# Performance work log

Hardware: AMD Instinct MI355X
Metric: run time of the kernel (lower is better)

Reference implementation:

```python
import jax, jax.numpy as jnp
import numpy as np
import math

NUM_HEADS = 16
TOPK = 64
EMBED = 1024

def setup_inputs() -> dict:
    key = jax.random.key(0)
    ks = jax.random.split(key, 11)
    b, s, e = 2, 2048, EMBED
    scale = 1.0 / math.sqrt(e)
    inp = {
        'q': jax.random.normal(ks[0], (b, s, e), dtype=jnp.float32),
        'k': jax.random.normal(ks[1], (b, s, e), dtype=jnp.float32),
        'v': jax.random.normal(ks[2], (b, s, e), dtype=jnp.float32),
        'Wq': jax.random.normal(ks[3], (e, e), dtype=jnp.float32) * scale,
        'bq': jnp.zeros((e,), dtype=jnp.float32),
        'Wk': jax.random.normal(ks[4], (e, e), dtype=jnp.float32) * scale,
        'bk': jnp.zeros((e,), dtype=jnp.float32),
        'Wv': jax.random.normal(ks[5], (e, e), dtype=jnp.float32) * scale,
        'bv': jnp.zeros((e,), dtype=jnp.float32),
        'Wo': jax.random.normal(ks[6], (e, e), dtype=jnp.float32) * scale,
        'bo': jnp.zeros((e,), dtype=jnp.float32),
    }
    return inp

def _topk_attention(Q, K, V, topk):
    # Q,K,V: (b, h, s, d)
    d = Q.shape[-1]
    scores = jnp.einsum('bhqd,bhkd->bhqk', Q, K) / jnp.sqrt(jnp.asarray(d, Q.dtype))
    topk_scores, topk_idx = jax.lax.top_k(scores, topk)  # (b,h,s,topk)
    probs = jax.nn.softmax(topk_scores, axis=-1)
    # gather V rows per (b,h): V_bh[idx] -> (s, topk, d); avoids (b,h,s,s,d) expand
    gather = jax.vmap(jax.vmap(lambda Vbh, idx: Vbh[idx]))
    sel = gather(V, topk_idx)  # (b,h,s,topk,d)
    return jnp.einsum('bhqk,bhqkd->bhqd', probs, sel)

def reference(q, k, v, Wq, bq, Wk, bk, Wv, bv, Wo, bo):
    b, s, e = q.shape
    h = NUM_HEADS
    d = e // h
    # NOTE: original torch code reshapes (b, s, e) -> (b, h, s, d) directly (no transpose)
    Q = (q @ Wq.T + bq).reshape(b, h, s, d)
    K = (k @ Wk.T + bk).reshape(b, h, s, d)
    V = (v @ Wv.T + bv).reshape(b, h, s, d)
    attn = _topk_attention(Q, K, V, TOPK)  # (b,h,s,d)
    out = attn.reshape(b, s, e)
    return out @ Wo.T + bo
```

## Files before the change

### kernel.cpp

```cpp
#include <hip/hip_runtime.h>
#include <stdint.h>

using u8  = unsigned char;
using s8  = signed char;
using u16 = unsigned short;
using u32 = unsigned int;
using u64 = unsigned long long;

typedef int   v4i __attribute__((ext_vector_type(4)));
typedef float v4f __attribute__((ext_vector_type(4)));
typedef short v8s __attribute__((ext_vector_type(8)));

__device__ __forceinline__ u16 f2bf(float f){
  u32 u = __builtin_bit_cast(u32, f);
  u32 r = (u + 0x7FFFu + ((u >> 16) & 1u)) >> 16;
  return (u16)r;
}
__device__ __forceinline__ float bf2f(u16 b){
  u32 u = ((u32)b) << 16;
  return __builtin_bit_cast(float, u);
}

__global__ __launch_bounds__(256) void quant_digits(
    const float* __restrict__ in, s8* __restrict__ dig, int n, float scale, float clampv)
{
  int t = blockIdx.x * 256 + threadIdx.x;
  int n8 = n >> 3;
  if (t >= n8) return;
  const float4* inv = (const float4*)in;
  float4 a = inv[2*t], b = inv[2*t+1];
  float xs[8] = {a.x,a.y,a.z,a.w,b.x,b.y,b.z,b.w};
  u64 p0=0,p1=0,p2=0,p3=0;
#pragma unroll
  for (int j=0;j<8;j++){
    float xv = fminf(fmaxf(xs[j], -clampv), clampv);
    int X = (int)rintf(xv * scale);
    int d0 = (int)(s8)(X & 255); X = (X - d0) >> 8;
    int d1 = (int)(s8)(X & 255); X = (X - d1) >> 8;
    int d2 = (int)(s8)(X & 255); X = (X - d2) >> 8;
    int d3 = X;
    p0 |= ((u64)(u8)(s8)d0) << (8*j);
    p1 |= ((u64)(u8)(s8)d1) << (8*j);
    p2 |= ((u64)(u8)(s8)d2) << (8*j);
    p3 |= ((u64)(u8)(s8)d3) << (8*j);
  }
  u64* o = (u64*)dig;
  size_t np8 = (size_t)n8;
  o[t] = p0; o[np8 + t] = p1; o[2*np8 + t] = p2; o[3*np8 + t] = p3;
}

#define MFMA_I8(c, a, b) asm volatile("v_mfma_i32_16x16x64_i8 %0, %1, %2, %0" : "+v"(c) : "v"(a), "v"(b))

__global__ __launch_bounds__(256) void gemm_i8(
    const s8* __restrict__ Ad, const s8* __restrict__ Wd, const float* __restrict__ bias,
    double* __restrict__ Cd, u16* __restrict__ Cb)
{
  __shared__ alignas(16) s8 As[4][64][80];
  __shared__ alignas(16) s8 Bs[4][64][80];
  const int i0 = blockIdx.x * 64, o0 = blockIdx.y * 64;
  const int t = threadIdx.x, w = t >> 6, lane = t & 63;
  const int wr = w >> 1, wc = w & 1, l15 = lane & 15, lg = lane >> 4;
  const int sr = (t >> 2) & 63, sc = (t & 3) << 4;
  const size_t APL = 4194304, WPL = 1048576;

  v4i acc[2][2][4];
#pragma unroll
  for (int tr = 0; tr < 2; ++tr)
#pragma unroll
    for (int tc = 0; tc < 2; ++tc)
#pragma unroll
      for (int c = 0; c < 4; ++c) acc[tr][tc][c] = (v4i){0,0,0,0};

  for (int kt = 0; kt < 16; ++kt){
#pragma unroll
    for (int p = 0; p < 4; ++p){
      int4 av = *(const int4*)(Ad + (size_t)p*APL + (size_t)(i0+sr)*1024 + kt*64 + sc);
      *(int4*)&As[p][sr][sc] = av;
      int4 bv = *(const int4*)(Wd + (size_t)p*WPL + (size_t)(o0+sr)*1024 + kt*64 + sc);
      *(int4*)&Bs[p][sr][sc] = bv;
    }
    __syncthreads();
    v4i af[2][4], bf[2][4];
#pragma unroll
    for (int tr = 0; tr < 2; ++tr)
#pragma unroll
      for (int p = 0; p < 4; ++p){
        af[tr][p] = *(const v4i*)&As[p][wr*32 + tr*16 + l15][lg*16];
        bf[tr][p] = *(const v4i*)&Bs[p][wc*32 + tr*16 + l15][lg*16];
      }
#pragma unroll
    for (int tr = 0; tr < 2; ++tr)
#pragma unroll
      for (int tc = 0; tc < 2; ++tc){
        MFMA_I8(acc[tr][tc][0], af[tr][0], bf[tc][3]);
        MFMA_I8(acc[tr][tc][0], af[tr][1], bf[tc][2]);
        MFMA_I8(acc[tr][tc][0], af[tr][2], bf[tc][1]);
        MFMA_I8(acc[tr][tc][0], af[tr][3], bf[tc][0]);
        MFMA_I8(acc[tr][tc][1], af[tr][1], bf[tc][3]);
        MFMA_I8(acc[tr][tc][1], af[tr][2], bf[tc][2]);
        MFMA_I8(acc[tr][tc][1], af[tr][3], bf[tc][1]);
        MFMA_I8(acc[tr][tc][2], af[tr][2], bf[tc][3]);
        MFMA_I8(acc[tr][tc][2], af[tr][3], bf[tc][2]);
        MFMA_I8(acc[tr][tc][3], af[tr][3], bf[tc][3]);
      }
    __syncthreads();
  }
#pragma unroll
  for (int tr = 0; tr < 2; ++tr)
#pragma unroll
    for (int tc = 0; tc < 2; ++tc){
      const int oc = o0 + wc*32 + tc*16 + l15;
      const double bv = (double)bias[oc];
#pragma unroll
      for (int e = 0; e < 4; ++e){
        double val = (double)acc[tr][tc][0][e]*0x1p-35 + (double)acc[tr][tc][1][e]*0x1p-27
                   + (double)acc[tr][tc][2][e]*0x1p-19 + (double)acc[tr][tc][3][e]*0x1p-11 + bv;
        int orow = i0 + wr*32 + tr*16 + lg*4 + e;
        size_t idx = (size_t)orow*1024 + oc;
        Cd[idx] = val;
        Cb[idx] = f2bf((float)val);
      }
    }
}

template<int ABF16, int OUTBF>
__global__ __launch_bounds__(256) void gemm_bf16k(
    const void* __restrict__ Ap, const float* __restrict__ W, const float* __restrict__ bias,
    void* __restrict__ C)
{
  __shared__ alignas(16) u16 As[64][72];
  __shared__ alignas(16) u16 Bs[64][72];
  const int i0 = blockIdx.x * 64, o0 = blockIdx.y * 64;
  const int t = threadIdx.x, w = t >> 6, lane = t & 63;
  const int wr = w >> 1, wc = w & 1, l15 = lane & 15, lg = lane >> 4;
  const int sr = t >> 2, sc = (t & 3) << 4;

  v4f acc[2][2];
#pragma unroll
  for (int tr = 0; tr < 2; ++tr)
#pragma unroll
    for (int tc = 0; tc < 2; ++tc) acc[tr][tc] = (v4f){0.f,0.f,0.f,0.f};

  for (int kt = 0; kt < 16; ++kt){
    if (ABF16){
      const u16* A = (const u16*)Ap;
      v8s x0 = *(const v8s*)(A + (size_t)(i0+sr)*1024 + kt*64 + sc);
      v8s x1 = *(const v8s*)(A + (size_t)(i0+sr)*1024 + kt*64 + sc + 8);
      *(v8s*)&As[sr][sc] = x0;
      *(v8s*)&As[sr][sc+8] = x1;
    } else {
      const float* A = (const float*)Ap;
      v8s pk0, pk1;
#pragma unroll
      for (int h = 0; h < 2; ++h){
        const float4 y0 = *(const float4*)(A + (size_t)(i0+sr)*1024 + kt*64 + sc + h*8);
        const float4 y1 = *(const float4*)(A + (size_t)(i0+sr)*1024 + kt*64 + sc + h*8 + 4);
        v8s& pk = h ? pk1 : pk0;
        pk[0]=(short)f2bf(y0.x); pk[1]=(short)f2bf(y0.y); pk[2]=(short)f2bf(y0.z); pk[3]=(short)f2bf(y0.w);
        pk[4]=(short)f2bf(y1.x); pk[5]=(short)f2bf(y1.y); pk[6]=(short)f2bf(y1.z); pk[7]=(short)f2bf(y1.w);
      }
      *(v8s*)&As[sr][sc] = pk0;
      *(v8s*)&As[sr][sc+8] = pk1;
    }
    {
      v8s pk0, pk1;
#pragma unroll
      for (int h = 0; h < 2; ++h){
        const float4 y0 = *(const float4*)(W + (size_t)(o0+sr)*1024 + kt*64 + sc + h*8);
        const float4 y1 = *(const float4*)(W + (size_t)(o0+sr)*1024 + kt*64 + sc + h*8 + 4);
        v8s& pk = h ? pk1 : pk0;
        pk[0]=(short)f2bf(y0.x); pk[1]=(short)f2bf(y0.y); pk[2]=(short)f2bf(y0.z); pk[3]=(short)f2bf(y0.w);
        pk[4]=(short)f2bf(y1.x); pk[5]=(short)f2bf(y1.y); pk[6]=(short)f2bf(y1.z); pk[7]=(short)f2bf(y1.w);
      }
      *(v8s*)&Bs[sr][sc] = pk0;
      *(v8s*)&Bs[sr][sc+8] = pk1;
    }
    __syncthreads();
    v8s a[2][2], b[2][2];
#pragma unroll
    for (int tr = 0; tr < 2; ++tr)
#pragma unroll
      for (int ks = 0; ks < 2; ++ks){
        a[tr][ks] = *(const v8s*)&As[wr*32 + tr*16 + l15][ks*32 + lg*8];
        b[tr][ks] = *(const v8s*)&Bs[wc*32 + tr*16 + l15][ks*32 + lg*8];
      }
#pragma unroll
    for (int tr = 0; tr < 2; ++tr)
#pragma unroll
      for (int tc = 0; tc < 2; ++tc){
        acc[tr][tc] = __builtin_amdgcn_mfma_f32_16x16x32_bf16(a[tr][0], b[tc][0], acc[tr][tc], 0, 0, 0);
        acc[tr][tc] = __builtin_amdgcn_mfma_f32_16x16x32_bf16(a[tr][1], b[tc][1], acc[tr][tc], 0, 0, 0);
      }
    __syncthreads();
  }
#pragma unroll
  for (int tr = 0; tr < 2; ++tr)
#pragma unroll
    for (int tc = 0; tc < 2; ++tc){
      const int oc = o0 + wc*32 + tc*16 + l15;
      const float bvv = bias[oc];
#pragma unroll
      for (int e = 0; e < 4; ++e){
        int orow = i0 + wr*32 + tr*16 + lg*4 + e;
        size_t idx = (size_t)orow*1024 + oc;
        if (OUTBF) ((u16*)C)[idx] = f2bf(acc[tr][tc][e] + bvv);
        else       ((float*)C)[idx] = acc[tr][tc][e] + bvv;
      }
    }
}

#define CCAP 192
__global__ __launch_bounds__(512, 4) void attn_topk(
    const u16* __restrict__ Qb, const u16* __restrict__ Kb,
    const double* __restrict__ Qd, const double* __restrict__ Kd,
    const u16* __restrict__ Vb, u16* __restrict__ Ab, u32* __restrict__ flags)
{
  __shared__ u32 candL[32*CCAP];
  __shared__ u32 selpL[16*64];
  __shared__ int cntA[32];

  const int lid = blockIdx.y * 64 + blockIdx.x;
  const int bh  = (lid & 7) * 4 + (lid >> 9);
  const int qb  = (lid >> 3) & 63;
  const size_t base = (size_t)(bh >> 4) * 2097152 + (size_t)(bh & 15) * 131072;
  const int q0 = qb * 32;
  const int tid = threadIdx.x, w = tid >> 6, lane = tid & 63;
  const int l15 = lane & 15, lg = lane >> 4;
  const u64 ltmask = (1ull << lane) - 1ull;

  if (tid < 32) cntA[tid] = 0;
  __syncthreads();

  const v4f vzero = {0.f,0.f,0.f,0.f};
  float nrmA, nrmB;
  {
    const size_t qoffA = base + (size_t)(q0 + l15)*64 + lg*8;
    v8s aA0 = *(const v8s*)(Qb + qoffA);
    v8s aA1 = *(const v8s*)(Qb + qoffA + 32);
    v8s aB0 = *(const v8s*)(Qb + qoffA + 1024);
    v8s aB1 = *(const v8s*)(Qb + qoffA + 1024 + 32);

    nrmA = 0.f; nrmB = 0.f;
#pragma unroll
    for (int m = 0; m < 8; ++m){
      float xA0 = bf2f((u16)aA0[m]), xA1 = bf2f((u16)aA1[m]);
      float xB0 = bf2f((u16)aB0[m]), xB1 = bf2f((u16)aB1[m]);
      nrmA = fmaf(xA0,xA0,nrmA); nrmA = fmaf(xA1,xA1,nrmA);
      nrmB = fmaf(xB0,xB0,nrmB); nrmB = fmaf(xB1,xB1,nrmB);
    }
    nrmA += __shfl_xor(nrmA,16); nrmA += __shfl_xor(nrmA,32);
    nrmB += __shfl_xor(nrmB,16); nrmB += __shfl_xor(nrmB,32);
    float T0A[4], T0B[4];
#pragma unroll
    for (int e = 0; e < 4; ++e){
      T0A[e] = 0.2f * sqrtf(__shfl(nrmA, lg*4 + e));
      T0B[e] = 0.2f * sqrtf(__shfl(nrmB, lg*4 + e));
    }

    const u16* Kw = Kb + base + (size_t)(w*256 + l15)*64 + lg*8;
    v8s b0 = *(const v8s*)(Kw);
    v8s b1 = *(const v8s*)(Kw + 32);

    auto step = [&](int kt, v8s b0c, v8s b1c){
      v4f sA = __builtin_amdgcn_mfma_f32_16x16x32_bf16(aA0, b0c, vzero, 0,0,0);
      sA = __builtin_amdgcn_mfma_f32_16x16x32_bf16(aA1, b1c, sA, 0,0,0);
      v4f sB = __builtin_amdgcn_mfma_f32_16x16x32_bf16(aB0, b0c, vzero, 0,0,0);
      sB = __builtin_amdgcn_mfma_f32_16x16x32_bf16(aB1, b1c, sB, 0,0,0);
      const u32 col = (u32)(w*256 + kt*16 + l15);
#pragma unroll
      for (int e = 0; e < 4; ++e){
        float sc = sA[e]*0.125f;
        if (sc >= T0A[e]){
          int row = lg*4 + e;
          int pos = atomicAdd(&cntA[row], 1);
          if (pos < CCAP) candL[row*CCAP + pos] = ((u32)f2bf(sc)<<16) | col;
        }
        float sc2 = sB[e]*0.125f;
        if (sc2 >= T0B[e]){
          int row = 16 + lg*4 + e;
          int pos = atomicAdd(&cntA[row], 1);
          if (pos < CCAP) candL[row*CCAP + pos] = ((u32)f2bf(sc2)<<16) | col;
        }
      }
    };

    for (int kt = 0; kt < 15; ++kt){
      v8s n0 = *(const v8s*)(Kw + (size_t)(kt+1)*1024);
      v8s n1 = *(const v8s*)(Kw + (size_t)(kt+1)*1024 + 32);
      step(kt, b0, b1);
      b0 = n0; b1 = n1;
    }
    step(15, b0, b1);
  }
  __syncthreads();

  for (int pass = 0; pass < 2; ++pass){
    const int R0 = pass*16 + w*2;
    const float nrmP0 = (pass == 0) ? nrmA : nrmB;
    u32 pk0[2], pk1[2], pk2[2], cstore[2], tv[2];
    bool fail[2];

#pragma unroll
    for (int rr = 0; rr < 2; ++rr){
      const int R = R0 + rr;
      int craw = cntA[R];
      fail[rr] = (craw > CCAP);
      cstore[rr] = (u32)(craw > CCAP ? CCAP : craw);
#pragma unroll
      for (int s = 0; s < 3; ++s){
        u32 idx = (u32)(64*s + lane);
        u32 val = (idx < cstore[rr]) ? candL[R*CCAP + idx] : 0u;
        if (s == 0) pk0[rr] = val; else if (s == 1) pk1[rr] = val; else pk2[rr] = val;
      }
      tv[rr] = 0u;
    }

    for (int bit = 14; bit >= 0; --bit){
#pragma unroll
      for (int rr = 0; rr < 2; ++rr){
        u32 tt = tv[rr] | (1u << bit);
        int c = (int)__popcll(__ballot((pk0[rr] >> 16) >= tt))
              + (int)__popcll(__ballot((pk1[rr] >> 16) >= tt))
              + (int)__popcll(__ballot((pk2[rr] >> 16) >= tt));
        if (c >= 64) tv[rr] = tt;
      }
    }

    int na[2], nb[2];
#pragma unroll
    for (int rr = 0; rr < 2; ++rr){
      const int R = R0 + rr;
      const int Rl = R & 15;
      float t64f = bf2f((u16)tv[rr]);
      float T0R = 0.2f * sqrtf(__shfl(nrmP0, R & 15));
      float thi = t64f + 0.052f, tlo = t64f - 0.052f;
      int a_ = 0, b_ = 0;
#pragma unroll
      for (int s = 0; s < 3; ++s){
        u32 pkv = (s == 0) ? pk0[rr] : ((s == 1) ? pk1[rr] : pk2[rr]);
        bool act = (u32)(64*s + lane) < cstore[rr];
        float v = bf2f((u16)(pkv >> 16));
        bool aut = act && (v > thi);
        bool ban = act && !aut && (v >= tlo);
        u64 ma = __ballot(aut);
        if (aut){
          int pos = a_ + (int)__popcll(ma & ltmask);
          if (pos < 64) selpL[Rl*64 + pos] = pkv;
        }
        a_ += (int)__popcll(ma);
        u64 mb = __ballot(ban);
        if (ban){
          int pos = b_ + (int)__popcll(mb & ltmask);
          if (pos < 64) candL[R*CCAP + pos] = pkv;
        }
        b_ += (int)__popcll(mb);
      }
      bool fl = fail[rr] || (t64f < T0R + 0.055f) || (t64f >= 3.98f) || (b_ > 64);
      fail[rr] = fl;
      if (lane == 0) flags[bh*2048 + q0 + R] = fl ? 1u : 0u;
      na[rr] = fl ? 64 : (a_ > 64 ? 64 : a_);
      nb[rr] = fl ? 0  : b_;
    }
    asm volatile("s_waitcnt lgkmcnt(0)" ::: "memory");
    __builtin_amdgcn_sched_barrier(0);

    const double* Kdh = Kd + base;
    const double* Qdh = Qd + base + (size_t)q0*64;
    u32 bpk[2];
#pragma unroll
    for (int rr = 0; rr < 2; ++rr)
      bpk[rr] = (lane < nb[rr]) ? candL[(R0+rr)*CCAP + lane] : 0u;
    double ac0[2] = {0,0}, ac1[2] = {0,0};
#pragma unroll 4
    for (int j = 0; j < 32; ++j){
#pragma unroll
      for (int rr = 0; rr < 2; ++rr){
        double2 kv = ((const double2*)(Kdh + (size_t)(bpk[rr] & 0x7FFu)*64))[j];
        double2 qv = ((const double2*)(Qdh + (size_t)(R0+rr)*64))[j];
        ac0[rr] = fma(qv.x, kv.x, ac0[rr]);
        ac1[rr] = fma(qv.y, kv.y, ac1[rr]);
      }
    }
    double mv[2]; int mi[2];
#pragma unroll
    for (int rr = 0; rr < 2; ++rr){
      mv[rr] = (lane < nb[rr]) ? (ac0[rr] + ac1[rr]) : -1.0e300;
      mi[rr] = (lane < nb[rr]) ? (int)(bpk[rr] & 0x7FFu) : 0x7FFFFFFF;
    }
    int maxnb = nb[0] > nb[1] ? nb[0] : nb[1];
    int rank[2] = {0,0};
    for (int j = 0; j < maxnb; ++j){
#pragma unroll
      for (int rr = 0; rr < 2; ++rr){
        double ov = __shfl(mv[rr], j); int oi = __shfl(mi[rr], j);
        rank[rr] += (ov > mv[rr] || (ov == mv[rr] && oi < mi[rr])) ? 1 : 0;
      }
    }
#pragma unroll
    for (int rr = 0; rr < 2; ++rr){
      int need = 64 - na[rr]; if (need > nb[rr]) need = nb[rr];
      if (lane < nb[rr] && rank[rr] < need)
        selpL[((R0+rr) & 15)*64 + na[rr] + rank[rr]] = bpk[rr];
    }
    asm volatile("s_waitcnt lgkmcnt(0)" ::: "memory");
    __builtin_amdgcn_sched_barrier(0);

    u32 sidx[2]; float scv[2], pp[2];
#pragma unroll
    for (int rr = 0; rr < 2; ++rr){
      u32 pr = selpL[((R0+rr) & 15)*64 + lane];
      sidx[rr] = pr & 0x7FFu;
      scv[rr] = __builtin_bit_cast(float, pr & 0xFFFF0000u);
    }
#pragma unroll
    for (int rr = 0; rr < 2; ++rr){
      float mx = scv[rr];
#pragma unroll
      for (int off = 32; off; off >>= 1) mx = fmaxf(mx, __shfl_xor(mx, off));
      float p = expf(scv[rr] - mx);
      float Z = p;
#pragma unroll
      for (int off = 32; off; off >>= 1) Z += __shfl_xor(Z, off);
      pp[rr] = p / Z;
    }
    u64 myp0 = ((u64)__builtin_bit_cast(u32, pp[0]) << 32) | (u64)sidx[0];
    u64 myp1 = ((u64)__builtin_bit_cast(u32, pp[1]) << 32) | (u64)sidx[1];

    const int h = lane >> 5, dl = lane & 31;
    float u0[2] = {0,0}, u1[2] = {0,0};
#pragma unroll 4
    for (int j = 0; j < 64; j += 2){
      u64 pr0 = __shfl(myp0, j + h);
      u64 pr1 = __shfl(myp1, j + h);
#pragma unroll
      for (int rr = 0; rr < 2; ++rr){
        u64 pr = (rr == 0) ? pr0 : pr1;
        float pv = __builtin_bit_cast(float, (u32)(pr >> 32));
        u32 vv = *(const u32*)(Vb + base + (size_t)((u32)pr & 0x7FFu)*64 + 2*dl);
        u0[rr] = fmaf(pv, bf2f((u16)(vv & 0xFFFFu)), u0[rr]);
        u1[rr] = fmaf(pv, bf2f((u16)(vv >> 16)),     u1[rr]);
      }
    }
#pragma unroll
    for (int rr = 0; rr < 2; ++rr){
      u0[rr] += __shfl_xor(u0[rr], 32);
      u1[rr] += __shfl_xor(u1[rr], 32);
    }
    if (lane < 32){
#pragma unroll
      for (int rr = 0; rr < 2; ++rr){
        u32 o = (u32)f2bf(u0[rr]) | ((u32)f2bf(u1[rr]) << 16);
        *(u32*)(Ab + base + (size_t)(q0 + R0 + rr)*64 + 2*dl) = o;
      }
    }
  }
}

__global__ __launch_bounds__(256) void attn_fallback(
    const u32* __restrict__ flags, const double* __restrict__ Qd,
    const double* __restrict__ Kd, const u16* __restrict__ Vb,
    u16* __restrict__ Ab)
{
  __shared__ double ktileL[4][16*64];
  __shared__ double valsL[2048];
  __shared__ double qlds[64];
  __shared__ double selvL[64];
  __shared__ int    seliL[64];
  __shared__ float  ppL[64];
  __shared__ float  ovL[4][64];
  __shared__ double redv[4];
  __shared__ int    redi[4];
  __shared__ double bcv;
  __shared__ int    bci;
  __shared__ u32    mskL;

  const int blk = blockIdx.x;
  const int tid = threadIdx.x, w = tid >> 6, lane = tid & 63;

  if (tid == 0){
    u32 m = 0;
    for (int i = 0; i < 16; ++i) m |= (flags[blk*16 + i] ? 1u : 0u) << i;
    mskL = m;
  }
  __syncthreads();
  const u32 msk = mskL;
  if (msk == 0u) return;

  for (int i = 0; i < 16; ++i){
    if (!((msk >> i) & 1u)) continue;
    const int g = blk*16 + i;
    const int bh = g >> 11, qrow = g & 2047;
    const size_t base = (size_t)(bh >> 4)*2097152 + (size_t)(bh & 15)*131072;
    if (tid < 64) qlds[tid] = Qd[base + (size_t)qrow*64 + tid];
    __syncthreads();

    double* ktw = ktileL[w];
    const int gg = lane >> 4, r = lane & 15;
    for (int t = 0; t < 32; ++t){
      const int k0 = w*512 + t*16;
#pragma unroll
      for (int r2 = 0; r2 < 16; ++r2)
        ktw[r2*64 + ((lane + r2) & 63)] = Kd[base + (size_t)(k0 + r2)*64 + lane];
      double p = 0.0;
#pragma unroll
      for (int dd = 0; dd < 16; ++dd){
        int d = gg*16 + dd;
        p = fma(qlds[d], ktw[r*64 + ((d + r) & 63)], p);
      }
      p += __shfl_xor(p, 16);
      p += __shfl_xor(p, 32);
      if (lane < 16) valsL[k0 + lane] = p * 0.125;
    }
    __syncthreads();

    double myv[8];
#pragma unroll
    for (int m2 = 0; m2 < 8; ++m2) myv[m2] = valsL[tid*8 + m2];

    double pvv = 1.0e300; int pii = -1;
    for (int step = 0; step < 64; ++step){
      double bv = -1.0e300; int bi = 0x7FFFFFFF;
#pragma unroll
      for (int m2 = 0; m2 < 8; ++m2){
        double vv = myv[m2]; int col = tid*8 + m2;
        bool after = (vv < pvv) || (vv == pvv && col > pii);
        bool bet = after && (vv > bv || (vv == bv && col < bi));
        bv = bet ? vv : bv; bi = bet ? col : bi;
      }
#pragma unroll
      for (int off = 32; off; off >>= 1){
        double ov = __shfl_xor(bv, off); int oi = __shfl_xor(bi, off);
        bool tk = (ov > bv) || (ov == bv && oi < bi);
        bv = tk ? ov : bv; bi = tk ? oi : bi;
      }
      if (lane == 0){ redv[w] = bv; redi[w] = bi; }
      __syncthreads();
      if (tid == 0){
        double fv = redv[0]; int fi = redi[0];
#pragma unroll
        for (int x = 1; x < 4; ++x){
          bool tk = (redv[x] > fv) || (redv[x] == fv && redi[x] < fi);
          fv = tk ? redv[x] : fv; fi = tk ? redi[x] : fi;
        }
        bcv = fv; bci = fi; selvL[step] = fv; seliL[step] = fi;
      }
      __syncthreads();
      pvv = bcv; pii = bci;
    }

    if (w == 0){
      float sc = (float)selvL[lane];
      float mx = sc;
#pragma unroll
      for (int off = 32; off; off >>= 1) mx = fmaxf(mx, __shfl_xor(mx, off));
      float p = expf(sc - mx);
      float Z = p;
#pragma unroll
      for (int off = 32; off; off >>= 1) Z += __shfl_xor(Z, off);
      ppL[lane] = p / Z;
    }
    __syncthreads();

    float o = 0.f;
#pragma unroll
    for (int j = 0; j < 16; ++j){
      int jj = w*16 + j;
      o = fmaf(ppL[jj], bf2f(Vb[base + (size_t)seliL[jj]*64 + lane]), o);
    }
    ovL[w][lane] = o;
    __syncthreads();
    if (w == 0){
      float oo = (ovL[0][lane] + ovL[1][lane]) + (ovL[2][lane] + ovL[3][lane]);
      Ab[base + (size_t)qrow*64 + lane] = f2bf(oo);
    }
    __syncthreads();
  }
}

extern "C" void kernel_launch(void* const* d_in, const int* in_sizes, int n_in,
                              void* d_out, int out_size, void* d_ws, size_t ws_size,
                              hipStream_t stream)
{
  (void)in_sizes; (void)n_in; (void)out_size; (void)ws_size;
  const float* q  = (const float*)d_in[0];
  const float* k  = (const float*)d_in[1];
  const float* v  = (const float*)d_in[2];
  const float* Wq = (const float*)d_in[3];
  const float* bq = (const float*)d_in[4];
  const float* Wk = (const float*)d_in[5];
  const float* bk = (const float*)d_in[6];
  const float* Wv = (const float*)d_in[7];
  const float* bv = (const float*)d_in[8];
  const float* Wo = (const float*)d_in[9];
  const float* bo = (const float*)d_in[10];

  char* ws = (char*)d_ws;
  const size_t MB = 1048576;
  double* Qd  = (double*)(ws);
  double* Kd  = (double*)(ws + 32*MB);
  u16*    Qb  = (u16*)  (ws + 64*MB);
  u16*    Kb  = (u16*)  (ws + 72*MB);
  u16*    Abf = (u16*)  (ws + 80*MB);
  s8*     dact= (s8*)   (ws + 88*MB);
  u16*    Vbf = (u16*)  (ws + 88*MB);
  s8*     dw  = (s8*)   (ws + 104*MB);
  u32*    flg = (u32*)  (ws + 104*MB);

  quant_digits<<<2048, 256, 0, stream>>>(q,  dact, 4194304, 134217728.0f, 7.75f);
  quant_digits<<<512,  256, 0, stream>>>(Wq, dw,   1048576, 4294967296.0f, 0.2495f);
  gemm_i8<<<dim3(64, 16), 256, 0, stream>>>(dact, dw, bq, Qd, Qb);
  quant_digits<<<2048, 256, 0, stream>>>(k,  dact, 4194304, 134217728.0f, 7.75f);
  quant_digits<<<512,  256, 0, stream>>>(Wk, dw,   1048576, 4294967296.0f, 0.2495f);
  gemm_i8<<<dim3(64, 16), 256, 0, stream>>>(dact, dw, bk, Kd, Kb);
  gemm_bf16k<0,1><<<dim3(64, 16), 256, 0, stream>>>(v, Wv, bv, Vbf);
  attn_topk<<<dim3(64, 32), 512, 0, stream>>>(Qb, Kb, Qd, Kd, Vbf, Abf, flg);
  attn_fallback<<<4096, 256, 0, stream>>>(flg, Qd, Kd, Vbf, Abf);
  gemm_bf16k<1,0><<<dim3(64, 16), 256, 0, stream>>>(Abf, Wo, bo, d_out);
}
```

Measured before the change: 588.4 us.

## Process 64 query rows per attention block to reuse each K tile more

The top-k attention kernel now handles 64 query rows per block instead of 32, holding four Q fragments in registers and running four MFMA groups against each loaded K tile. The grid is halved and the selection phase loops over four passes. The aim is to amortise K loads over more queries. In exchange it uses more registers and LDS (the candidate buffer grows even with a slightly smaller per-row cap), which may cut occupancy, and the smaller cap could push more rows into the fallback path.

```diff
diff --git a/kernel.cpp b/kernel.cpp
--- a/kernel.cpp
+++ b/kernel.cpp
@@ -209,52 +209,51 @@
     }
 }
 
-#define CCAP 192
+#define CCAP 184
 __global__ __launch_bounds__(512, 4) void attn_topk(
     const u16* __restrict__ Qb, const u16* __restrict__ Kb,
     const double* __restrict__ Qd, const double* __restrict__ Kd,
     const u16* __restrict__ Vb, u16* __restrict__ Ab, u32* __restrict__ flags)
 {
-  __shared__ u32 candL[32*CCAP];
+  __shared__ u32 candL[64*CCAP];
   __shared__ u32 selpL[16*64];
-  __shared__ int cntA[32];
-
-  const int lid = blockIdx.y * 64 + blockIdx.x;
-  const int bh  = (lid & 7) * 4 + (lid >> 9);
-  const int qb  = (lid >> 3) & 63;
+  __shared__ int cntA[64];
+
+  const int lid = blockIdx.y * 32 + blockIdx.x;
+  const int bh  = (lid & 7) * 4 + (lid >> 8);
+  const int qb  = (lid >> 3) & 31;
   const size_t base = (size_t)(bh >> 4) * 2097152 + (size_t)(bh & 15) * 131072;
-  const int q0 = qb * 32;
+  const int q0 = qb * 64;
   const int tid = threadIdx.x, w = tid >> 6, lane = tid & 63;
   const int l15 = lane & 15, lg = lane >> 4;
   const u64 ltmask = (1ull << lane) - 1ull;
 
-  if (tid < 32) cntA[tid] = 0;
+  if (tid < 64) cntA[tid] = 0;
   __syncthreads();
 
   const v4f vzero = {0.f,0.f,0.f,0.f};
-  float nrmA, nrmB;
+  float nrm0, nrm1, nrm2, nrm3;
   {
-    const size_t qoffA = base + (size_t)(q0 + l15)*64 + lg*8;
-    v8s aA0 = *(const v8s*)(Qb + qoffA);
-    v8s aA1 = *(const v8s*)(Qb + qoffA + 32);
-    v8s aB0 = *(const v8s*)(Qb + qoffA + 1024);
-    v8s aB1 = *(const v8s*)(Qb + qoffA + 1024 + 32);
-
-    nrmA = 0.f; nrmB = 0.f;
-#pragma unroll
-    for (int m = 0; m < 8; ++m){
-      float xA0 = bf2f((u16)aA0[m]), xA1 = bf2f((u16)aA1[m]);
-      float xB0 = bf2f((u16)aB0[m]), xB1 = bf2f((u16)aB1[m]);
-      nrmA = fmaf(xA0,xA0,nrmA); nrmA = fmaf(xA1,xA1,nrmA);
-      nrmB = fmaf(xB0,xB0,nrmB); nrmB = fmaf(xB1,xB1,nrmB);
-    }
-    nrmA += __shfl_xor(nrmA,16); nrmA += __shfl_xor(nrmA,32);
-    nrmB += __shfl_xor(nrmB,16); nrmB += __shfl_xor(nrmB,32);
-    float T0A[4], T0B[4];
-#pragma unroll
-    for (int e = 0; e < 4; ++e){
-      T0A[e] = 0.2f * sqrtf(__shfl(nrmA, lg*4 + e));
-      T0B[e] = 0.2f * sqrtf(__shfl(nrmB, lg*4 + e));
+    v8s aQ[4][2];
+    float T0v[4][4];
+#pragma unroll
+    for (int g = 0; g < 4; ++g){
+      const size_t qoff = base + (size_t)(q0 + g*16 + l15)*64 + lg*8;
+      aQ[g][0] = *(const v8s*)(Qb + qoff);
+      aQ[g][1] = *(const v8s*)(Qb + qoff + 32);
+      float nr = 0.f;
+#pragma unroll
+      for (int m = 0; m < 8; ++m){
+        float x0 = bf2f((u16)aQ[g][0][m]), x1 = bf2f((u16)aQ[g][1][m]);
+        nr = fmaf(x0,x0,nr); nr = fmaf(x1,x1,nr);
+      }
+      nr += __shfl_xor(nr,16);
+      nr += __shfl_xor(nr,32);
+      if (g == 0) nrm0 = nr; else if (g == 1) nrm1 = nr;
+      else if (g == 2) nrm2 = nr; else nrm3 = nr;
+#pragma unroll
+      for (int e = 0; e < 4; ++e)
+        T0v[g][e] = 0.2f * sqrtf(__shfl(nr, lg*4 + e));
     }
 
     const u16* Kw = Kb + base + (size_t)(w*256 + l15)*64 + lg*8;
@@ -262,24 +261,19 @@
     v8s b1 = *(const v8s*)(Kw + 32);
 
     auto step = [&](int kt, v8s b0c, v8s b1c){
-      v4f sA = __builtin_amdgcn_mfma_f32_16x16x32_bf16(aA0, b0c, vzero, 0,0,0);
-      sA = __builtin_amdgcn_mfma_f32_16x16x32_bf16(aA1, b1c, sA, 0,0,0);
-      v4f sB = __builtin_amdgcn_mfma_f32_16x16x32_bf16(aB0, b0c, vzero, 0,0,0);
-      sB = __builtin_amdgcn_mfma_f32_16x16x32_bf16(aB1, b1c, sB, 0,0,0);
       const u32 col = (u32)(w*256 + kt*16 + l15);
 #pragma unroll
-      for (int e = 0; e < 4; ++e){
-        float sc = sA[e]*0.125f;
-        if (sc >= T0A[e]){
-          int row = lg*4 + e;
-          int pos = atomicAdd(&cntA[row], 1);
-          if (pos < CCAP) candL[row*CCAP + pos] = ((u32)f2bf(sc)<<16) | col;
-        }
-        float sc2 = sB[e]*0.125f;
-        if (sc2 >= T0B[e]){
-          int row = 16 + lg*4 + e;
-          int pos = atomicAdd(&cntA[row], 1);
-          if (pos < CCAP) candL[row*CCAP + pos] = ((u32)f2bf(sc2)<<16) | col;
+      for (int g = 0; g < 4; ++g){
+        v4f s = __builtin_amdgcn_mfma_f32_16x16x32_bf16(aQ[g][0], b0c, vzero, 0,0,0);
+        s = __builtin_amdgcn_mfma_f32_16x16x32_bf16(aQ[g][1], b1c, s, 0,0,0);
+#pragma unroll
+        for (int e = 0; e < 4; ++e){
+          float sc = s[e]*0.125f;
+          if (sc >= T0v[g][e]){
+            int row = g*16 + lg*4 + e;
+            int pos = atomicAdd(&cntA[row], 1);
+            if (pos < CCAP) candL[row*CCAP + pos] = ((u32)f2bf(sc)<<16) | col;
+          }
         }
       }
     };
@@ -294,9 +288,9 @@
   }
   __syncthreads();
 
-  for (int pass = 0; pass < 2; ++pass){
+  for (int pass = 0; pass < 4; ++pass){
     const int R0 = pass*16 + w*2;
-    const float nrmP0 = (pass == 0) ? nrmA : nrmB;
+    const float nrmP = (pass == 0) ? nrm0 : ((pass == 1) ? nrm1 : ((pass == 2) ? nrm2 : nrm3));
     u32 pk0[2], pk1[2], pk2[2], cstore[2], tv[2];
     bool fail[2];
 
@@ -309,7 +303,7 @@
 #pragma unroll
       for (int s = 0; s < 3; ++s){
         u32 idx = (u32)(64*s + lane);
-        u32 val = (idx < cstore[rr]) ? candL[R*CCAP + idx] : 0u;
+        u32 val = (idx < cstore[rr] && idx < CCAP) ? candL[R*CCAP + idx] : 0u;
         if (s == 0) pk0[rr] = val; else if (s == 1) pk1[rr] = val; else pk2[rr] = val;
       }
       tv[rr] = 0u;
@@ -332,7 +326,7 @@
       const int R = R0 + rr;
       const int Rl = R & 15;
       float t64f = bf2f((u16)tv[rr]);
-      float T0R = 0.2f * sqrtf(__shfl(nrmP0, R & 15));
+      float T0R = 0.2f * sqrtf(__shfl(nrmP, R & 15));
       float thi = t64f + 0.052f, tlo = t64f - 0.052f;
       int a_ = 0, b_ = 0;
 #pragma unroll
@@ -613,7 +607,7 @@
   quant_digits<<<512,  256, 0, stream>>>(Wk, dw,   1048576, 4294967296.0f, 0.2495f);
   gemm_i8<<<dim3(64, 16), 256, 0, stream>>>(dact, dw, bk, Kd, Kb);
   gemm_bf16k<0,1><<<dim3(64, 16), 256, 0, stream>>>(v, Wv, bv, Vbf);
-  attn_topk<<<dim3(64, 32), 512, 0, stream>>>(Qb, Kb, Qd, Kd, Vbf, Abf, flg);
+  attn_topk<<<dim3(32, 32), 512, 0, stream>>>(Qb, Kb, Qd, Kd, Vbf, Abf, flg);
   attn_fallback<<<4096, 256, 0, stream>>>(flg, Qd, Kd, Vbf, Abf);
   gemm_bf16k<1,0><<<dim3(64, 16), 256, 0, stream>>>(Abf, Wo, bo, d_out);
 }
```

New measurement: 570.4 us. -3.1%, faster.
